# Kernel optimization log

Hardware: AMD Instinct MI355X
Metric: run time of the kernel (lower is better)

Reference implementation:

```python
import jax, jax.numpy as jnp
import numpy as np
import math

B, L, S, E, D = 32, 2048, 2048, 64, 64

def setup_inputs() -> dict:
    key = jax.random.key(0)
    kq, kk, kv = jax.random.split(key, 3)
    return {
        "queries": jax.random.normal(kq, (B, L, E), dtype=jnp.float32),
        "keys":    jax.random.normal(kk, (B, S, E), dtype=jnp.float32),
        "values":  jax.random.normal(kv, (B, S, D), dtype=jnp.float32),
    }

def reference(queries, keys, values):
    # scale = 1/sqrt(E) since self.scale is None
    scale = 1.0 / math.sqrt(queries.shape[-1])
    # unfused QK^T -> softmax -> V (dropout is identity at inference)
    scores = jnp.einsum('ble,bse->bls', queries, keys)  # [B,L,S]
    # mask_flag branch not taken because L == S (matches torch code path)
    A = jax.nn.softmax(scale * scores, axis=-1)
    V = jnp.einsum('bls,bsd->bld', A, values)  # [B,L,D]
    return V
```

## Files before the change

kernel.cpp:

```cpp
#include <hip/hip_runtime.h>
#include <hip/hip_bf16.h>


#define B_ 32
#define L_ 2048
#define S_ 2048
#define E_ 64
#define D_ 64
#define BQ 128
#define NIMG 32
#define IMG_BYTES 16384
#define NCHUNK 16

typedef __attribute__((ext_vector_type(8))) short bf16x8;
typedef __attribute__((ext_vector_type(16))) float f32x16;
typedef __attribute__((ext_vector_type(4))) unsigned u32x4;

__device__ __forceinline__ unsigned short f2b(float f) {
  unsigned u = __builtin_bit_cast(unsigned, f);
  u += 0x7fff + ((u >> 16) & 1);
  return (unsigned short)(u >> 16);
}

__device__ __forceinline__ unsigned pk2(float a, float b) {
#if defined(__has_builtin) && __has_builtin(__builtin_amdgcn_cvt_pk_bf16_f32)
  typedef __bf16 b2 __attribute__((ext_vector_type(2)));
  b2 t = __builtin_amdgcn_cvt_pk_bf16_f32(a, b);
  return __builtin_bit_cast(unsigned, t);
#else
  return (unsigned)f2b(a) | ((unsigned)f2b(b) << 16);
#endif
}

__device__ __forceinline__ float fexp2(float x) {
#if defined(__has_builtin) && __has_builtin(__builtin_amdgcn_exp2f)
  return __builtin_amdgcn_exp2f(x);
#else
  return exp2f(x);
#endif
}

__device__ __forceinline__ void cp16(const void* g, void* lbase) {
#if defined(__has_builtin) && __has_builtin(__builtin_amdgcn_global_load_lds)
  typedef const __attribute__((address_space(1))) void gvoid;
  typedef __attribute__((address_space(3))) void lvoid;
  __builtin_amdgcn_global_load_lds((gvoid*)g, (lvoid*)lbase, 16, 0, 0);
#endif
}

__global__ __launch_bounds__(256) void prepass(
    const float* __restrict__ K, const float* __restrict__ V,
    char* __restrict__ ws) {
  __shared__ __align__(16) short vimg[4096];

  const int tid  = threadIdx.x;
  const int lane = tid & 63;
  const int quad = lane >> 4;
  const int qb0  = quad & 1;
  const int qb1  = (quad >> 1) & 1;

  const int b  = blockIdx.x >> 5;
  const int c  = blockIdx.x & 31;
  const int s0 = c * 64;

  const float* Kb = K + (long)b * S_ * E_;
  const float* Vb = V + (long)b * S_ * D_;
  short* img = (short*)(ws + (size_t)blockIdx.x * IMG_BYTES);

#pragma unroll
  for (int it = 0; it < 4; ++it) {
    const int i  = tid + it * 256;
    const int s  = i >> 4;
    const int c4 = (i & 15) << 2;

    float4 kv = *(const float4*)(Kb + (long)(s0 + s) * E_ + c4);
    {
      int g = (c4 >> 3) ^ (s & 7);
      *(uint2*)&img[s * 64 + g * 8 + (c4 & 7)] = make_uint2(pk2(kv.x, kv.y), pk2(kv.z, kv.w));
    }

    float4 vv = *(const float4*)(Vb + (long)(s0 + s) * D_ + c4);
    float a0 = vv.x, a1 = vv.y, a2 = vv.z, a3 = vv.w;
    float s0f = qb1 ? a0 : a2;
    float s1f = qb1 ? a1 : a3;
    float r0  = __shfl_xor(s0f, 32);
    float r1  = __shfl_xor(s1f, 32);
    float b0 = qb1 ? r0 : a0;
    float b1 = qb1 ? r1 : a1;
    float b2 = qb1 ? a2 : r0;
    float b3 = qb1 ? a3 : r1;
    float t0 = qb0 ? b0 : b1;
    float t1 = qb0 ? b2 : b3;
    float u0 = __shfl_xor(t0, 16);
    float u1 = __shfl_xor(t1, 16);
    float w0 = qb0 ? u0 : b0;
    float w1 = qb0 ? b1 : u0;
    float w2 = qb0 ? u1 : b2;
    float w3 = qb0 ? b3 : u1;
    const int base = s - quad;
    const int d    = c4 + quad;
    int g = (base >> 3) ^ (d & 7);
    *(uint2*)&vimg[d * 64 + g * 8 + (base & 7)] = make_uint2(pk2(w0, w1), pk2(w2, w3));
  }

  __syncthreads();

  {
    const char* src = (const char*)vimg + tid * 32;
    char* dst = (char*)img + 8192 + tid * 32;
    *(float4*)(dst)      = *(const float4*)(src);
    *(float4*)(dst + 16) = *(const float4*)(src + 16);
  }
}

__global__ __launch_bounds__(512, 4) void attn_fwd(
    const float* __restrict__ Q, const char* __restrict__ ws,
    float* __restrict__ O) {
  __shared__ __align__(16) char smem[65536 + 1024];
  float* Obuf = (float*)smem;
  float* ML   = (float*)(smem + 65536);

  const int tid  = threadIdx.x;
  const int lane = tid & 63;
  const int wv   = tid >> 6;
  const int l31  = lane & 31;
  const int h    = lane >> 5;
  const int qg   = wv >> 1;
  const int kh   = wv & 1;

  const int i_ = blockIdx.x;
  const int x_ = i_ & 7;
  const int j_ = i_ >> 3;
  const int b  = (x_ << 2) | (j_ >> 4);
  const int q0 = (j_ & 15) * BQ;

  const float SCALE2 = 0.125f * 1.44269504088896340736f;
  const char* img0 = ws + (size_t)b * ((size_t)NIMG * IMG_BYTES);

  bf16x8 qf[4];
  {
    const float* qrow = Q + ((long)b * L_ + q0 + qg * 32 + l31) * E_;
#pragma unroll
    for (int ke = 0; ke < 4; ++ke) {
      const float* sp = qrow + ke * 16 + h * 8;
      float4 x = *(const float4*)(sp);
      float4 y = *(const float4*)(sp + 4);
      u32x4 uu = { pk2(x.x * SCALE2, x.y * SCALE2), pk2(x.z * SCALE2, x.w * SCALE2),
                   pk2(y.x * SCALE2, y.y * SCALE2), pk2(y.z * SCALE2, y.w * SCALE2) };
      qf[ke] = __builtin_bit_cast(bf16x8, uu);
    }
  }

#pragma unroll
  for (int j = 0; j < 4; ++j)
    cp16(img0 + wv * 4096 + j * 1024 + lane * 16, smem + wv * 4096 + j * 1024);

  int pl = l31;
  {
    const int blk = (pl >> 2) & 3;
    if (blk == 1) pl += 4;
    else if (blk == 2) pl -= 4;
  }

  const int kb = kh * 16384 + (pl << 7) + ((h ^ (pl & 7)) << 4);
  const int vb = kh * 16384 + 8192 + (l31 << 7) + ((h ^ (l31 & 7)) << 4);

  f32x16 o[2];
#pragma unroll
  for (int mt = 0; mt < 2; ++mt)
#pragma unroll
    for (int r = 0; r < 16; ++r) o[mt][r] = 0.f;
  float lrun = 0.f;

#define CHUNK_BODY(TT, BUFB, OTHB)                                             \
  {                                                                            \
    if ((TT) + 1 < NCHUNK) {                                                   \
      const char* img = img0 + (size_t)((TT) + 1) * 32768;                     \
      _Pragma("unroll")                                                        \
      for (int j = 0; j < 4; ++j)                                              \
        cp16(img + wv * 4096 + j * 1024 + lane * 16,                           \
             smem + (OTHB) + wv * 4096 + j * 1024);                            \
      asm volatile("s_waitcnt vmcnt(4)" ::: "memory");                         \
    } else {                                                                   \
      asm volatile("s_waitcnt vmcnt(0)" ::: "memory");                         \
    }                                                                          \
    __builtin_amdgcn_s_barrier();            \
    __builtin_amdgcn_sched_barrier(0);                                         \
    _Pragma("unroll")                                                          \
    for (int nt = 0; nt < 2; ++nt) {                                           \
      bf16x8 kf[4];                                                            \
      _Pragma("unroll")                                                        \
      for (int ke = 0; ke < 4; ++ke)                                           \
        kf[ke] = *(const bf16x8*)(smem +                                       \
                   (kb ^ ((BUFB) | (nt << 12) | (ke << 5))));                  \
      f32x16 acc;                                                              \
      _Pragma("unroll")                                                        \
      for (int r = 0; r < 16; ++r) acc[r] = 0.f;                               \
      __builtin_amdgcn_s_setprio(1);                                           \
      _Pragma("unroll")                                                        \
      for (int ke = 0; ke < 4; ++ke)                                           \
        acc = __builtin_amdgcn_mfma_f32_32x32x16_bf16(kf[ke], qf[ke], acc,     \
                                                      0, 0, 0);                \
      __builtin_amdgcn_s_setprio(0);                                           \
      u32x4 f0, f1;                                                            \
      _Pragma("unroll")                                                        \
      for (int gixx = 0; gixx < 4; ++gixx) {                                   \
        float p0 = fexp2(acc[2 * gixx]);                                       \
        float p1 = fexp2(acc[2 * gixx + 1]);                                   \
        float p2 = fexp2(acc[8 + 2 * gixx]);                                   \
        float p3 = fexp2(acc[8 + 2 * gixx + 1]);                               \
        f0[gixx] = pk2(p0, p1);                                                \
        f1[gixx] = pk2(p2, p3);                                                \
        lrun += (p0 + p1) + (p2 + p3);                                         \
      }                                                                        \
      bf16x8 pf0 = __builtin_bit_cast(bf16x8, f0);                             \
      bf16x8 pf1 = __builtin_bit_cast(bf16x8, f1);                             \
      __builtin_amdgcn_s_setprio(1);                                           \
      _Pragma("unroll")                                                        \
      for (int mt = 0; mt < 2; ++mt) {                                         \
        bf16x8 vf0 = *(const bf16x8*)(smem +                                   \
                      (vb ^ ((BUFB) | (mt << 12) | ((nt * 2 + 0) << 5))));     \
        o[mt] = __builtin_amdgcn_mfma_f32_32x32x16_bf16(vf0, pf0, o[mt],       \
                                                        0, 0, 0);              \
        bf16x8 vf1 = *(const bf16x8*)(smem +                                   \
                      (vb ^ ((BUFB) | (mt << 12) | ((nt * 2 + 1) << 5))));     \
        o[mt] = __builtin_amdgcn_mfma_f32_32x32x16_bf16(vf1, pf1, o[mt],       \
                                                        0, 0, 0);              \
      }                                                                        \
      __builtin_amdgcn_s_setprio(0);                                           \
    }                                                                          \
    __builtin_amdgcn_s_barrier();              \
  }

  for (int t = 0; t < NCHUNK; t += 2) {
    CHUNK_BODY(t, 0, 32768)
    CHUNK_BODY(t + 1, 32768, 0)
  }
#undef CHUNK_BODY

  float lt = lrun + __shfl_xor(lrun, 32);

  if (lane < 32)
    ML[(qg * 2 + kh) * 32 + l31] = lt;
  __syncthreads();

  const float inv = 1.f / (lt + ML[(qg * 2 + (kh ^ 1)) * 32 + l31]);
  const int q = qg * 32 + l31;

  if (kh == 1) {
#pragma unroll
    for (int mt = 0; mt < 2; ++mt)
#pragma unroll
      for (int r = 0; r < 16; ++r) {
        const int d = mt * 32 + (r & 3) + 8 * (r >> 2) + 4 * h;
        Obuf[q * 68 + d] = o[mt][r];
      }
  }
  __syncthreads();

  if (kh == 0) {
#pragma unroll
    for (int mt = 0; mt < 2; ++mt)
#pragma unroll
      for (int r = 0; r < 16; ++r) {
        const int d = mt * 32 + (r & 3) + 8 * (r >> 2) + 4 * h;
        Obuf[q * 68 + d] = (o[mt][r] + Obuf[q * 68 + d]) * inv;
      }
  }
  __syncthreads();

  {
    const int qq = tid >> 2;
    const int dh = (tid & 3) * 16;
    float* orow = O + ((long)b * L_ + q0 + qq) * D_ + dh;
    const float* src = &Obuf[qq * 68 + dh];
#pragma unroll
    for (int j = 0; j < 4; ++j)
      *(float4*)(orow + j * 4) = *(const float4*)(src + j * 4);
  }
}

extern "C" void kernel_launch(void* const* d_in, const int* in_sizes, int n_in,
                              void* d_out, int out_size, void* d_ws, size_t ws_size,
                              hipStream_t stream) {
  const float* Q = (const float*)d_in[0];
  const float* K = (const float*)d_in[1];
  const float* V = (const float*)d_in[2];
  float* O = (float*)d_out;

  prepass<<<dim3(B_ * NIMG), dim3(256), 0, stream>>>(K, V, (char*)d_ws);
  attn_fwd<<<dim3(B_ * (L_ / BQ)), dim3(512), 0, stream>>>(Q, (const char*)d_ws, O);
}
```

Before: 138.1 us.

## Double query tile per block so each wave reuses K/V fragments across two query tiles

Raises the query tile to 256 rows per block, so each wave now computes two 32-row query tiles against each K/V fragment loaded from LDS. This halves the number of blocks and roughly halves the K/V LDS reads and global image copies per query row. The inner loop is restructured by hand to interleave the QK MFMAs, the exp, and the PV MFMAs across the two tiles. In exchange, register pressure roughly doubles (occupancy hint lowered from 4 to 2 blocks), LDS grows for the larger output buffer, and the grid gets coarser.

Result: no change. 137.4 us (-0.5%).

```diff
diff --git a/kernel.cpp b/kernel.cpp
--- a/kernel.cpp
+++ b/kernel.cpp
@@ -7,7 +7,7 @@
 #define S_ 2048
 #define E_ 64
 #define D_ 64
-#define BQ 128
+#define BQ 256
 #define NIMG 32
 #define IMG_BYTES 16384
 #define NCHUNK 16
@@ -113,47 +113,58 @@
   }
 }
 
-__global__ __launch_bounds__(512, 4) void attn_fwd(
+__global__ __launch_bounds__(512, 2) void attn_fwd(
     const float* __restrict__ Q, const char* __restrict__ ws,
     float* __restrict__ O) {
-  __shared__ __align__(16) char smem[65536 + 1024];
+  __shared__ __align__(16) char smem[71680];
   float* Obuf = (float*)smem;
-  float* ML   = (float*)(smem + 65536);
+  float* ML   = (float*)(smem + 69632);
 
   const int tid  = threadIdx.x;
   const int lane = tid & 63;
   const int wv   = tid >> 6;
   const int l31  = lane & 31;
   const int h    = lane >> 5;
-  const int qg   = wv >> 1;
+  const int qt   = wv >> 1;
   const int kh   = wv & 1;
 
   const int i_ = blockIdx.x;
   const int x_ = i_ & 7;
   const int j_ = i_ >> 3;
-  const int b  = (x_ << 2) | (j_ >> 4);
-  const int q0 = (j_ & 15) * BQ;
+  const int b  = (x_ << 2) | (j_ >> 3);
+  const int q0 = (j_ & 7) * BQ;
 
   const float SCALE2 = 0.125f * 1.44269504088896340736f;
   const char* img0 = ws + (size_t)b * ((size_t)NIMG * IMG_BYTES);
 
-  bf16x8 qf[4];
+  bf16x8 qf0[4], qf1[4];
   {
-    const float* qrow = Q + ((long)b * L_ + q0 + qg * 32 + l31) * E_;
+    const float* qrow0 = Q + ((long)b * L_ + q0 + qt * 64 + l31) * E_;
 #pragma unroll
     for (int ke = 0; ke < 4; ++ke) {
-      const float* sp = qrow + ke * 16 + h * 8;
+      const float* sp = qrow0 + ke * 16 + h * 8;
       float4 x = *(const float4*)(sp);
       float4 y = *(const float4*)(sp + 4);
       u32x4 uu = { pk2(x.x * SCALE2, x.y * SCALE2), pk2(x.z * SCALE2, x.w * SCALE2),
                    pk2(y.x * SCALE2, y.y * SCALE2), pk2(y.z * SCALE2, y.w * SCALE2) };
-      qf[ke] = __builtin_bit_cast(bf16x8, uu);
-    }
-  }
+      qf0[ke] = __builtin_bit_cast(bf16x8, uu);
+    }
+    const float* qrow1 = qrow0 + 32 * E_;
+#pragma unroll
+    for (int ke = 0; ke < 4; ++ke) {
+      const float* sp = qrow1 + ke * 16 + h * 8;
+      float4 x = *(const float4*)(sp);
+      float4 y = *(const float4*)(sp + 4);
+      u32x4 uu = { pk2(x.x * SCALE2, x.y * SCALE2), pk2(x.z * SCALE2, x.w * SCALE2),
+                   pk2(y.x * SCALE2, y.y * SCALE2), pk2(y.z * SCALE2, y.w * SCALE2) };
+      qf1[ke] = __builtin_bit_cast(bf16x8, uu);
+    }
+  }
+  __builtin_amdgcn_sched_barrier(0);
 
 #pragma unroll
   for (int j = 0; j < 4; ++j)
-    cp16(img0 + wv * 4096 + j * 1024 + lane * 16, smem + wv * 4096 + j * 1024);
+    cp16(img0 + j * 8192 + tid * 16, smem + j * 8192 + tid * 16);
 
   int pl = l31;
   {
@@ -162,15 +173,35 @@
     else if (blk == 2) pl -= 4;
   }
 
-  const int kb = kh * 16384 + (pl << 7) + ((h ^ (pl & 7)) << 4);
-  const int vb = kh * 16384 + 8192 + (l31 << 7) + ((h ^ (l31 & 7)) << 4);
-
-  f32x16 o[2];
-#pragma unroll
-  for (int mt = 0; mt < 2; ++mt)
-#pragma unroll
-    for (int r = 0; r < 16; ++r) o[mt][r] = 0.f;
-  float lrun = 0.f;
+  const int kbse = kh * 16384 + (pl << 7) + ((h ^ (pl & 7)) << 4);
+  const int vbse = kh * 16384 + 8192 + (l31 << 7) + ((h ^ (l31 & 7)) << 4);
+
+#define LDK(BUFB, NT, KE) \
+  (*(const bf16x8*)(smem + (kbse ^ ((BUFB) | ((NT) << 12) | ((KE) << 5)))))
+#define LDV(BUFB, MT, KS) \
+  (*(const bf16x8*)(smem + (vbse ^ ((BUFB) | ((MT) << 12) | ((KS) << 5)))))
+#define MF(A, B, C) __builtin_amdgcn_mfma_f32_32x32x16_bf16(A, B, C, 0, 0, 0)
+
+#define EXP16(ACC, PF0, PF1, LR) {                                             \
+    u32x4 f0_, f1_;                                                            \
+    _Pragma("unroll")                                                          \
+    for (int g_ = 0; g_ < 4; ++g_) {                                           \
+      float p0 = fexp2(ACC[2 * g_]);                                           \
+      float p1 = fexp2(ACC[2 * g_ + 1]);                                       \
+      float p2 = fexp2(ACC[8 + 2 * g_]);                                       \
+      float p3 = fexp2(ACC[8 + 2 * g_ + 1]);                                   \
+      f0_[g_] = pk2(p0, p1);                                                   \
+      f1_[g_] = pk2(p2, p3);                                                   \
+      LR += (p0 + p1) + (p2 + p3);                                             \
+    }                                                                          \
+    PF0 = __builtin_bit_cast(bf16x8, f0_);                                     \
+    PF1 = __builtin_bit_cast(bf16x8, f1_);                                     \
+  }
+
+  f32x16 o00, o01, o10, o11;
+#pragma unroll
+  for (int r = 0; r < 16; ++r) { o00[r] = 0.f; o01[r] = 0.f; o10[r] = 0.f; o11[r] = 0.f; }
+  float lrun0 = 0.f, lrun1 = 0.f;
 
 #define CHUNK_BODY(TT, BUFB, OTHB)                                             \
   {                                                                            \
@@ -178,58 +209,60 @@
       const char* img = img0 + (size_t)((TT) + 1) * 32768;                     \
       _Pragma("unroll")                                                        \
       for (int j = 0; j < 4; ++j)                                              \
-        cp16(img + wv * 4096 + j * 1024 + lane * 16,                           \
-             smem + (OTHB) + wv * 4096 + j * 1024);                            \
+        cp16(img + j * 8192 + tid * 16, smem + (OTHB) + j * 8192 + tid * 16);  \
       asm volatile("s_waitcnt vmcnt(4)" ::: "memory");                         \
     } else {                                                                   \
       asm volatile("s_waitcnt vmcnt(0)" ::: "memory");                         \
     }                                                                          \
-    __builtin_amdgcn_s_barrier();            \
+    __builtin_amdgcn_s_barrier();                                              \
     __builtin_amdgcn_sched_barrier(0);                                         \
+                               \
+    bf16x8 ka0 = LDK(BUFB, 0, 0), ka1 = LDK(BUFB, 0, 1),                       \
+           ka2 = LDK(BUFB, 0, 2), ka3 = LDK(BUFB, 0, 3);                       \
+    f32x16 aA0, aA1;                                                           \
     _Pragma("unroll")                                                          \
-    for (int nt = 0; nt < 2; ++nt) {                                           \
-      bf16x8 kf[4];                                                            \
-      _Pragma("unroll")                                                        \
-      for (int ke = 0; ke < 4; ++ke)                                           \
-        kf[ke] = *(const bf16x8*)(smem +                                       \
-                   (kb ^ ((BUFB) | (nt << 12) | (ke << 5))));                  \
-      f32x16 acc;                                                              \
-      _Pragma("unroll")                                                        \
-      for (int r = 0; r < 16; ++r) acc[r] = 0.f;                               \
-      __builtin_amdgcn_s_setprio(1);                                           \
-      _Pragma("unroll")                                                        \
-      for (int ke = 0; ke < 4; ++ke)                                           \
-        acc = __builtin_amdgcn_mfma_f32_32x32x16_bf16(kf[ke], qf[ke], acc,     \
-                                                      0, 0, 0);                \
-      __builtin_amdgcn_s_setprio(0);                                           \
-      u32x4 f0, f1;                                                            \
-      _Pragma("unroll")                                                        \
-      for (int gixx = 0; gixx < 4; ++gixx) {                                   \
-        float p0 = fexp2(acc[2 * gixx]);                                       \
-        float p1 = fexp2(acc[2 * gixx + 1]);                                   \
-        float p2 = fexp2(acc[8 + 2 * gixx]);                                   \
-        float p3 = fexp2(acc[8 + 2 * gixx + 1]);                               \
-        f0[gixx] = pk2(p0, p1);                                                \
-        f1[gixx] = pk2(p2, p3);                                                \
-        lrun += (p0 + p1) + (p2 + p3);                                         \
-      }                                                                        \
-      bf16x8 pf0 = __builtin_bit_cast(bf16x8, f0);                             \
-      bf16x8 pf1 = __builtin_bit_cast(bf16x8, f1);                             \
-      __builtin_amdgcn_s_setprio(1);                                           \
-      _Pragma("unroll")                                                        \
-      for (int mt = 0; mt < 2; ++mt) {                                         \
-        bf16x8 vf0 = *(const bf16x8*)(smem +                                   \
-                      (vb ^ ((BUFB) | (mt << 12) | ((nt * 2 + 0) << 5))));     \
-        o[mt] = __builtin_amdgcn_mfma_f32_32x32x16_bf16(vf0, pf0, o[mt],       \
-                                                        0, 0, 0);              \
-        bf16x8 vf1 = *(const bf16x8*)(smem +                                   \
-                      (vb ^ ((BUFB) | (mt << 12) | ((nt * 2 + 1) << 5))));     \
-        o[mt] = __builtin_amdgcn_mfma_f32_32x32x16_bf16(vf1, pf1, o[mt],       \
-                                                        0, 0, 0);              \
-      }                                                                        \
-      __builtin_amdgcn_s_setprio(0);                                           \
+    for (int r = 0; r < 16; ++r) { aA0[r] = 0.f; aA1[r] = 0.f; }               \
+    aA0 = MF(ka0, qf0[0], aA0); aA1 = MF(ka0, qf1[0], aA1);                    \
+    aA0 = MF(ka1, qf0[1], aA0); aA1 = MF(ka1, qf1[1], aA1);                    \
+    aA0 = MF(ka2, qf0[2], aA0); aA1 = MF(ka2, qf1[2], aA1);                    \
+    aA0 = MF(ka3, qf0[3], aA0); aA1 = MF(ka3, qf1[3], aA1);                    \
+                                                               \
+    bf16x8 kc0 = LDK(BUFB, 1, 0), kc1 = LDK(BUFB, 1, 1),                       \
+           kc2 = LDK(BUFB, 1, 2), kc3 = LDK(BUFB, 1, 3);                       \
+    f32x16 aB0, aB1;                                                           \
+    _Pragma("unroll")                                                          \
+    for (int r = 0; r < 16; ++r) { aB0[r] = 0.f; aB1[r] = 0.f; }               \
+    aB0 = MF(kc0, qf0[0], aB0); aB1 = MF(kc0, qf1[0], aB1);                    \
+    aB0 = MF(kc1, qf0[1], aB0); aB1 = MF(kc1, qf1[1], aB1);                    \
+    aB0 = MF(kc2, qf0[2], aB0); aB1 = MF(kc2, qf1[2], aB1);                    \
+    aB0 = MF(kc3, qf0[3], aB0); aB1 = MF(kc3, qf1[3], aB1);                    \
+                              \
+    bf16x8 pA00, pA01, pA10, pA11;                                             \
+    EXP16(aA0, pA00, pA01, lrun0);                                             \
+    EXP16(aA1, pA10, pA11, lrun1);                                             \
+                         \
+    {                                                                          \
+      bf16x8 v00 = LDV(BUFB, 0, 0), v10 = LDV(BUFB, 1, 0),                     \
+             v01 = LDV(BUFB, 0, 1), v11 = LDV(BUFB, 1, 1);                     \
+      o00 = MF(v00, pA00, o00); o01 = MF(v10, pA00, o01);                      \
+      o10 = MF(v00, pA10, o10); o11 = MF(v10, pA10, o11);                      \
+      o00 = MF(v01, pA01, o00); o01 = MF(v11, pA01, o01);                      \
+      o10 = MF(v01, pA11, o10); o11 = MF(v11, pA11, o11);                      \
     }                                                                          \
-    __builtin_amdgcn_s_barrier();              \
+                              \
+    bf16x8 pB00, pB01, pB10, pB11;                                             \
+    EXP16(aB0, pB00, pB01, lrun0);                                             \
+    EXP16(aB1, pB10, pB11, lrun1);                                             \
+                                                       \
+    {                                                                          \
+      bf16x8 v02 = LDV(BUFB, 0, 2), v12 = LDV(BUFB, 1, 2),                     \
+             v03 = LDV(BUFB, 0, 3), v13 = LDV(BUFB, 1, 3);                     \
+      o00 = MF(v02, pB00, o00); o01 = MF(v12, pB00, o01);                      \
+      o10 = MF(v02, pB10, o10); o11 = MF(v12, pB10, o11);                      \
+      o00 = MF(v03, pB01, o00); o01 = MF(v13, pB01, o01);                      \
+      o10 = MF(v03, pB11, o10); o11 = MF(v13, pB11, o11);                      \
+    }                                                                          \
+    __builtin_amdgcn_s_barrier();                                              \
   }
 
   for (int t = 0; t < NCHUNK; t += 2) {
@@ -238,44 +271,50 @@
   }
 #undef CHUNK_BODY
 
-  float lt = lrun + __shfl_xor(lrun, 32);
-
-  if (lane < 32)
-    ML[(qg * 2 + kh) * 32 + l31] = lt;
+  float lt0 = lrun0 + __shfl_xor(lrun0, 32);
+  float lt1 = lrun1 + __shfl_xor(lrun1, 32);
+
+  if (lane < 32) {
+    ML[(qt * 2 + kh) * 64 + l31]      = lt0;
+    ML[(qt * 2 + kh) * 64 + 32 + l31] = lt1;
+  }
   __syncthreads();
 
-  const float inv = 1.f / (lt + ML[(qg * 2 + (kh ^ 1)) * 32 + l31]);
-  const int q = qg * 32 + l31;
+  const float inv0 = 1.f / (lt0 + ML[(qt * 2 + (kh ^ 1)) * 64 + l31]);
+  const float inv1 = 1.f / (lt1 + ML[(qt * 2 + (kh ^ 1)) * 64 + 32 + l31]);
+  const int qrow = qt * 64 + l31;
 
   if (kh == 1) {
 #pragma unroll
-    for (int mt = 0; mt < 2; ++mt)
-#pragma unroll
-      for (int r = 0; r < 16; ++r) {
-        const int d = mt * 32 + (r & 3) + 8 * (r >> 2) + 4 * h;
-        Obuf[q * 68 + d] = o[mt][r];
-      }
+    for (int r = 0; r < 16; ++r) {
+      const int d = (r & 3) + 8 * (r >> 2) + 4 * h;
+      Obuf[qrow * 68 + d]             = o00[r];
+      Obuf[qrow * 68 + 32 + d]        = o01[r];
+      Obuf[(qrow + 32) * 68 + d]      = o10[r];
+      Obuf[(qrow + 32) * 68 + 32 + d] = o11[r];
+    }
   }
   __syncthreads();
 
   if (kh == 0) {
 #pragma unroll
-    for (int mt = 0; mt < 2; ++mt)
-#pragma unroll
-      for (int r = 0; r < 16; ++r) {
-        const int d = mt * 32 + (r & 3) + 8 * (r >> 2) + 4 * h;
-        Obuf[q * 68 + d] = (o[mt][r] + Obuf[q * 68 + d]) * inv;
-      }
+    for (int r = 0; r < 16; ++r) {
+      const int d = (r & 3) + 8 * (r >> 2) + 4 * h;
+      Obuf[qrow * 68 + d]             = (o00[r] + Obuf[qrow * 68 + d]) * inv0;
+      Obuf[qrow * 68 + 32 + d]        = (o01[r] + Obuf[qrow * 68 + 32 + d]) * inv0;
+      Obuf[(qrow + 32) * 68 + d]      = (o10[r] + Obuf[(qrow + 32) * 68 + d]) * inv1;
+      Obuf[(qrow + 32) * 68 + 32 + d] = (o11[r] + Obuf[(qrow + 32) * 68 + 32 + d]) * inv1;
+    }
   }
   __syncthreads();
 
   {
-    const int qq = tid >> 2;
-    const int dh = (tid & 3) * 16;
+    const int qq = tid >> 1;
+    const int dh = (tid & 1) * 32;
     float* orow = O + ((long)b * L_ + q0 + qq) * D_ + dh;
     const float* src = &Obuf[qq * 68 + dh];
 #pragma unroll
-    for (int j = 0; j < 4; ++j)
+    for (int j = 0; j < 8; ++j)
       *(float4*)(orow + j * 4) = *(const float4*)(src + j * 4);
   }
 }
```
